# Kernel optimization log

Hardware: AMD Instinct MI355X
Metric: run time of the kernel (lower is better)

Reference implementation:

```python
import jax, jax.numpy as jnp
import numpy as np

N_PRED = 29
F_DIM = 8192
H1 = 256
H2 = 128


def setup_inputs() -> dict:
    key = jax.random.key(0)
    ks = jax.random.split(key, 7)
    features = jax.random.normal(ks[0], (4096, F_DIM), dtype=jnp.float32)
    # Stacked per-predicate MLP weights (PyTorch Linear init scale ~ 1/sqrt(fan_in))
    W1 = jax.random.normal(ks[1], (N_PRED, F_DIM, H1), dtype=jnp.float32) / np.sqrt(F_DIM)
    b1 = jax.random.normal(ks[2], (N_PRED, H1), dtype=jnp.float32) / np.sqrt(F_DIM)
    W2 = jax.random.normal(ks[3], (N_PRED, H1, H2), dtype=jnp.float32) / np.sqrt(H1)
    b2 = jax.random.normal(ks[4], (N_PRED, H2), dtype=jnp.float32) / np.sqrt(H1)
    W3 = jax.random.normal(ks[5], (N_PRED, H2), dtype=jnp.float32) / np.sqrt(H2)
    b3 = jax.random.normal(ks[6], (N_PRED,), dtype=jnp.float32) / np.sqrt(H2)
    return {"features": features, "W1": W1, "b1": b1, "W2": W2, "b2": b2, "W3": W3, "b3": b3}


def reference(features, W1, b1, W2, b2, W3, b3):
    # 29 parallel heads as one batched (grouped) GEMM chain; dropout = identity (eval).
    h1 = jax.nn.relu(jnp.einsum('bf,pfh->bph', features, W1) + b1[None])   # [B, P, H1]
    h2 = jax.nn.relu(jnp.einsum('bph,phk->bpk', h1, W2) + b2[None])        # [B, P, H2]
    logits = jnp.einsum('bpk,pk->bp', h2, W3) + b3[None]                   # [B, P]
    return jax.nn.sigmoid(logits)
```

## Files before the change

kernel.cpp:

```cpp
#include <hip/hip_runtime.h>
#include <hip/hip_bf16.h>

typedef __attribute__((ext_vector_type(8))) short short8_t;
typedef __attribute__((ext_vector_type(8))) __bf16 bf16x8;
typedef __attribute__((ext_vector_type(4))) float f32x4;

__device__ __forceinline__ void gload16(const void* g, void* l) {
  __builtin_amdgcn_global_load_lds(
      (const __attribute__((address_space(1))) void*)g,
      (__attribute__((address_space(3))) void*)l, 16, 0, 0);
}

__device__ __forceinline__ unsigned short f2bf(float f) {
  __hip_bfloat16 h = __float2bfloat16(f);
  return __builtin_bit_cast(unsigned short, h);
}

#define BARRIER() asm volatile("s_barrier" ::: "memory")


__global__ void k_cvt_feat(const float* __restrict__ in, unsigned short* __restrict__ out) {
  const size_t N = (size_t)4096 * 8192;
  size_t i = ((size_t)blockIdx.x * 256 + threadIdx.x) * 4;
  const size_t stride = (size_t)gridDim.x * 256 * 4;
  for (; i < N; i += stride) {
    float4 v = *(const float4*)(in + i);
    ushort4 o;
    o.x = f2bf(v.x); o.y = f2bf(v.y); o.z = f2bf(v.z); o.w = f2bf(v.w);
    *(ushort4*)(out + i) = o;
  }
}

__global__ void k_cvt_w1(const float* __restrict__ W1, unsigned short* __restrict__ out, int p0) {
  __shared__ unsigned short t[64][262];
  const int p = p0 + blockIdx.z;
  const float* src = W1 + (size_t)p * 8192 * 256;
  unsigned short* dst = out + (size_t)blockIdx.z * 256 * 8192;
  const int f0 = blockIdx.x * 256, h0 = blockIdx.y * 64;
#pragma unroll
  for (int i = 0; i < 64; ++i) {
    int tt = i * 256 + threadIdx.x;
    int f = tt >> 6, c = tt & 63;
    t[c][f] = f2bf(src[(size_t)(f0 + f) * 256 + h0 + c]);
  }
  __syncthreads();
#pragma unroll
  for (int i = 0; i < 8; ++i) {
    int tt = i * 256 + threadIdx.x;
    int r = tt >> 5;
    int c8 = (tt & 31) * 8;
    short8_t o;
#pragma unroll
    for (int j = 0; j < 8; ++j) o[j] = (short)t[r][c8 + j];
    *(short8_t*)&dst[(size_t)(h0 + r) * 8192 + f0 + c8] = o;
  }
}

__global__ void k_cvt_w2(const float* __restrict__ W2, unsigned short* __restrict__ out) {
  const int p = blockIdx.x;
  const float* src = W2 + (size_t)p * 256 * 128;
  unsigned short* dst = out + (size_t)p * 128 * 256;
  for (int tt = threadIdx.x; tt < 128 * 256; tt += 256) {
    int j = tt >> 8, h = tt & 255;
    dst[tt] = f2bf(src[(size_t)h * 128 + j]);
  }
}

__global__ __launch_bounds__(512, 2) void k_gemm1(
    const unsigned short* __restrict__ A,
    const unsigned short* __restrict__ Bt,
    const float* __restrict__ b1,
    const unsigned short* __restrict__ W2t,
    const float* __restrict__ b2,
    const float* __restrict__ W3,
    const float* __restrict__ b3,
    float* __restrict__ out,
    int p0) {
  __shared__ __align__(16) unsigned short S[65536];

  const int tid = threadIdx.x;
  const int lane = tid & 63;
  const int wave = tid >> 6;
  const int sr = (wave >> 2) * 64;
  const int sc = (wave & 3) * 32;

  const int nwg = gridDim.x * gridDim.y;
  const int orig = blockIdx.y * gridDim.x + blockIdx.x;
  const int q = nwg >> 3, r_ = nwg & 7;
  const int xcd = orig & 7, idx = orig >> 3;
  const int wg = (xcd < r_ ? xcd * (q + 1) : r_ * (q + 1) + (xcd - r_) * q) + idx;
  const int mx = wg & 15;
  const int z = wg >> 4;
  const int p = p0 + z;
  const int m0 = mx * 256;

  const unsigned short* Ab = A + (size_t)m0 * 8192;
  const unsigned short* Bb = Bt + (size_t)z * 256 * 8192;

  int e0 = tid, r0 = e0 >> 3, u0 = (e0 & 7) ^ (r0 & 7);
  int e1 = 512 + tid, r1e = e1 >> 3, u1 = (e1 & 7) ^ (r1e & 7);
  const size_t s0 = (size_t)r0 * 8192 + u0 * 8;
  const size_t s1 = (size_t)r1e * 8192 + u1 * 8;
  const int ld0 = (wave * 64) * 8;
  const int ld1 = (512 + wave * 64) * 8;

  auto stage = [&](int buf, int isB, int h, int T) {
    const unsigned short* gb = (isB ? Bb : Ab) + (size_t)h * 128 * 8192 + (size_t)T * 64;
    unsigned short* lb = S + buf * 32768 + isB * 16384 + h * 8192;
    gload16(gb + s0, lb + ld0);
    gload16(gb + s1, lb + ld1);
  };

  const int l15 = lane & 15, ks = lane >> 4;

  auto rdA = [&](int buf, int h, int mi, int x) {
    int R = sr + mi * 16 + l15;
    int pu = (x * 4 + ks) ^ (R & 7);
    return __builtin_bit_cast(bf16x8, *(const short8_t*)(S + buf * 32768 + h * 8192 + R * 64 + pu * 8));
  };
  auto rdB = [&](int buf, int v, int nj, int x) {
    int R = sc + nj * 16 + l15;
    int pu = (x * 4 + ks) ^ (R & 7);
    return __builtin_bit_cast(bf16x8, *(const short8_t*)(S + buf * 32768 + 16384 + v * 8192 + R * 64 + pu * 8));
  };

  f32x4 acc[4][4][2] = {};
  bf16x8 aH0[4][2], aH1[4][2], blf[2][2], bhf[2][2];
  const int NT = 8192 / 64;

  auto kstep = [&](int t, int pfa, int pf, int ra, int vm) {
    const int c = t & 1, nx = c ^ 1;
    BARRIER();
#pragma unroll
    for (int nj = 0; nj < 2; ++nj) { bhf[nj][0] = rdB(c, 1, nj, 0); bhf[nj][1] = rdB(c, 1, nj, 1); }
    if (pfa) stage(nx, 0, 1, t + 1);
    __builtin_amdgcn_s_setprio(1);
#pragma unroll
    for (int mi = 0; mi < 4; ++mi)
#pragma unroll
      for (int nj = 0; nj < 2; ++nj) {
        acc[0][mi][nj] = __builtin_amdgcn_mfma_f32_16x16x32_bf16(aH0[mi][0], blf[nj][0], acc[0][mi][nj], 0, 0, 0);
        acc[0][mi][nj] = __builtin_amdgcn_mfma_f32_16x16x32_bf16(aH0[mi][1], blf[nj][1], acc[0][mi][nj], 0, 0, 0);
      }
    __builtin_amdgcn_s_setprio(0);
    BARRIER();
#pragma unroll
    for (int mi = 0; mi < 4; ++mi) { aH1[mi][0] = rdA(c, 1, mi, 0); aH1[mi][1] = rdA(c, 1, mi, 1); }
    if (pf) stage(c, 0, 0, t + 2);
    __builtin_amdgcn_s_setprio(1);
#pragma unroll
    for (int mi = 0; mi < 4; ++mi)
#pragma unroll
      for (int nj = 0; nj < 2; ++nj) {
        acc[1][mi][nj] = __builtin_amdgcn_mfma_f32_16x16x32_bf16(aH0[mi][0], bhf[nj][0], acc[1][mi][nj], 0, 0, 0);
        acc[1][mi][nj] = __builtin_amdgcn_mfma_f32_16x16x32_bf16(aH0[mi][1], bhf[nj][1], acc[1][mi][nj], 0, 0, 0);
      }
    __builtin_amdgcn_s_setprio(0);
    BARRIER();
    if (pf) stage(c, 1, 1, t + 2);
    __builtin_amdgcn_s_setprio(1);
#pragma unroll
    for (int mi = 0; mi < 4; ++mi)
#pragma unroll
      for (int nj = 0; nj < 2; ++nj) {
        acc[2][mi][nj] = __builtin_amdgcn_mfma_f32_16x16x32_bf16(aH1[mi][0], blf[nj][0], acc[2][mi][nj], 0, 0, 0);
        acc[2][mi][nj] = __builtin_amdgcn_mfma_f32_16x16x32_bf16(aH1[mi][1], blf[nj][1], acc[2][mi][nj], 0, 0, 0);
      }
    __builtin_amdgcn_s_setprio(0);
    BARRIER();
    if (pf) stage(c, 1, 0, t + 2);
    if (vm == 6)      asm volatile("s_waitcnt vmcnt(6)" ::: "memory");
    else if (vm == 0) asm volatile("s_waitcnt vmcnt(0)" ::: "memory");
    BARRIER();
    if (ra) {
#pragma unroll
      for (int mi = 0; mi < 4; ++mi) { aH0[mi][0] = rdA(nx, 0, mi, 0); aH0[mi][1] = rdA(nx, 0, mi, 1); }
#pragma unroll
      for (int nj = 0; nj < 2; ++nj) { blf[nj][0] = rdB(nx, 0, nj, 0); blf[nj][1] = rdB(nx, 0, nj, 1); }
    }
    __builtin_amdgcn_s_setprio(1);
#pragma unroll
    for (int mi = 0; mi < 4; ++mi)
#pragma unroll
      for (int nj = 0; nj < 2; ++nj) {
        acc[3][mi][nj] = __builtin_amdgcn_mfma_f32_16x16x32_bf16(aH1[mi][0], bhf[nj][0], acc[3][mi][nj], 0, 0, 0);
        acc[3][mi][nj] = __builtin_amdgcn_mfma_f32_16x16x32_bf16(aH1[mi][1], bhf[nj][1], acc[3][mi][nj], 0, 0, 0);
      }
    __builtin_amdgcn_s_setprio(0);
  };

  stage(0, 0, 0, 0); stage(0, 1, 0, 0); stage(0, 1, 1, 0); stage(0, 0, 1, 0);
  stage(1, 0, 0, 1); stage(1, 1, 1, 1); stage(1, 1, 0, 1);
  asm volatile("s_waitcnt vmcnt(6)" ::: "memory");
  BARRIER();
#pragma unroll
  for (int mi = 0; mi < 4; ++mi) { aH0[mi][0] = rdA(0, 0, mi, 0); aH0[mi][1] = rdA(0, 0, mi, 1); }
#pragma unroll
  for (int nj = 0; nj < 2; ++nj) { blf[nj][0] = rdB(0, 0, nj, 0); blf[nj][1] = rdB(0, 0, nj, 1); }

  for (int t = 0; t < NT - 2; ++t) kstep(t, 1, 1, 1, 6);
  kstep(NT - 2, 1, 0, 1, 0);
  kstep(NT - 1, 0, 0, 0, -1);

  __syncthreads();
  {
    const int rg = lane >> 4;
#pragma unroll
    for (int qh = 0; qh < 2; ++qh)
#pragma unroll
      for (int qv = 0; qv < 2; ++qv) {
        const int qq = qh * 2 + qv;
#pragma unroll
        for (int nj = 0; nj < 2; ++nj) {
          const int c = qv * 128 + sc + nj * 16 + l15;
          const float bb = b1[p * 256 + c];
          const int u = c >> 3, sub = c & 7;
#pragma unroll
          for (int mi = 0; mi < 4; ++mi) {
            const int Rb = qh * 128 + sr + mi * 16 + rg * 4;
#pragma unroll
            for (int rr = 0; rr < 4; ++rr) {
              const int R = Rb + rr;
              float v = acc[qq][mi][nj][rr] + bb;
              v = v > 0.f ? v : 0.f;
              S[R * 256 + ((u ^ (R & 7)) * 8) + sub] = f2bf(v);
            }
          }
        }
      }
  }
  __syncthreads();
  {
    const unsigned short* Wp = W2t + (size_t)p * 128 * 256;
    f32x4 acc2[2][8] = {};
    bf16x8 bcur[8], bnxt[8];
#pragma unroll
    for (int nj = 0; nj < 8; ++nj)
      bcur[nj] = __builtin_bit_cast(bf16x8, *(const short8_t*)(Wp + (nj * 16 + l15) * 256 + ks * 8));
#pragma unroll
    for (int kt = 0; kt < 8; ++kt) {
      if (kt < 7) {
#pragma unroll
        for (int nj = 0; nj < 8; ++nj)
          bnxt[nj] = __builtin_bit_cast(bf16x8, *(const short8_t*)(Wp + (nj * 16 + l15) * 256 + (kt + 1) * 32 + ks * 8));
      }
      bf16x8 a2[2];
#pragma unroll
      for (int mi = 0; mi < 2; ++mi) {
        const int R = wave * 32 + mi * 16 + l15;
        const int u = kt * 4 + ks;
        a2[mi] = __builtin_bit_cast(bf16x8, *(const short8_t*)(S + R * 256 + ((u ^ (R & 7)) * 8)));
      }
#pragma unroll
      for (int mi = 0; mi < 2; ++mi)
#pragma unroll
        for (int nj = 0; nj < 8; ++nj)
          acc2[mi][nj] = __builtin_amdgcn_mfma_f32_16x16x32_bf16(a2[mi], bcur[nj], acc2[mi][nj], 0, 0, 0);
#pragma unroll
      for (int nj = 0; nj < 8; ++nj) bcur[nj] = bnxt[nj];
    }
    float b2v[8], w3v[8];
#pragma unroll
    for (int nj = 0; nj < 8; ++nj) {
      int c = nj * 16 + l15;
      b2v[nj] = b2[p * 128 + c];
      w3v[nj] = W3[p * 128 + c];
    }
    const float b3p = b3[p];
#pragma unroll
    for (int mi = 0; mi < 2; ++mi) {
#pragma unroll
      for (int r = 0; r < 4; ++r) {
        float s = 0.f;
#pragma unroll
        for (int nj = 0; nj < 8; ++nj) {
          float v = acc2[mi][nj][r] + b2v[nj];
          v = v > 0.f ? v : 0.f;
          s += v * w3v[nj];
        }
        s += __shfl_xor(s, 1);
        s += __shfl_xor(s, 2);
        s += __shfl_xor(s, 4);
        s += __shfl_xor(s, 8);
        if (l15 == 0) {
          int m = m0 + wave * 32 + mi * 16 + ks * 4 + r;
          float logit = s + b3p;
          out[(size_t)m * 29 + p] = 1.f / (1.f + __expf(-logit));
        }
      }
    }
  }
}

extern "C" void kernel_launch(void* const* d_in, const int* in_sizes, int n_in,
                              void* d_out, int out_size, void* d_ws, size_t ws_size,
                              hipStream_t stream) {
  const float* features = (const float*)d_in[0];
  const float* W1 = (const float*)d_in[1];
  const float* b1 = (const float*)d_in[2];
  const float* W2 = (const float*)d_in[3];
  const float* b2 = (const float*)d_in[4];
  const float* W3 = (const float*)d_in[5];
  const float* b3 = (const float*)d_in[6];
  float* out = (float*)d_out;

  char* ws = (char*)d_ws;
  const size_t featB = (size_t)4096 * 8192 * 2;
  const size_t w2B   = (size_t)29 * 128 * 256 * 2;
  const size_t w1pp  = (size_t)256 * 8192 * 2;

  unsigned short* featbf = (unsigned short*)ws;
  unsigned short* w2t    = (unsigned short*)(ws + featB);
  unsigned short* w1t    = (unsigned short*)(ws + featB + w2B);

  size_t base = featB + w2B;
  size_t rem = (ws_size > base) ? (ws_size - base) : 0;
  int CH = (int)(rem / w1pp);
  if (CH > 29) CH = 29;
  if (CH < 1) CH = 1;

  k_cvt_feat<<<2048, 256, 0, stream>>>(features, featbf);
  k_cvt_w2<<<29, 256, 0, stream>>>(W2, w2t);

  for (int p0 = 0; p0 < 29; p0 += CH) {
    int c = (29 - p0) < CH ? (29 - p0) : CH;
    k_cvt_w1<<<dim3(32, 4, c), 256, 0, stream>>>(W1, w1t, p0);
    k_gemm1<<<dim3(16, c), 512, 0, stream>>>(featbf, w1t, b1, w2t, b2, W3, b3, out, p0);
  }
}
```

Measured before the change: 531.8 us.

## Switch layer-1 GEMM to 32x32x16 MFMA with k-major LDS layout

Replaces the 16x16x32 bf16 MFMA tiles in the main W1 GEMM with 32x32x16 MFMA, which cuts the instruction count and raises operand reuse per instruction. The LDS staging layout changes from a row-major XOR-swizzled layout to a k-chunk-major layout so that 32-row fragments can be read contiguously. The epilogue is rewritten to match the 32x32 accumulator register mapping. The unswizzled layout may bring LDS bank conflicts on writes or reads, and the strided global loads may coalesce less well.

```diff
diff --git a/kernel.cpp b/kernel.cpp
--- a/kernel.cpp
+++ b/kernel.cpp
@@ -4,6 +4,7 @@
 typedef __attribute__((ext_vector_type(8))) short short8_t;
 typedef __attribute__((ext_vector_type(8))) __bf16 bf16x8;
 typedef __attribute__((ext_vector_type(4))) float f32x4;
+typedef __attribute__((ext_vector_type(16))) float f32x16;
 
 __device__ __forceinline__ void gload16(const void* g, void* l) {
   __builtin_amdgcn_global_load_lds(
@@ -97,8 +98,8 @@
   const unsigned short* Ab = A + (size_t)m0 * 8192;
   const unsigned short* Bb = Bt + (size_t)z * 256 * 8192;
 
-  int e0 = tid, r0 = e0 >> 3, u0 = (e0 & 7) ^ (r0 & 7);
-  int e1 = 512 + tid, r1e = e1 >> 3, u1 = (e1 & 7) ^ (r1e & 7);
+  int e0 = tid, u0 = e0 >> 7, r0 = e0 & 127;
+  int e1 = 512 + tid, u1 = e1 >> 7, r1e = e1 & 127;
   const size_t s0 = (size_t)r0 * 8192 + u0 * 8;
   const size_t s1 = (size_t)r1e * 8192 + u1 * 8;
   const int ld0 = (wave * 64) * 8;
@@ -112,60 +113,57 @@
   };
 
   const int l15 = lane & 15, ks = lane >> 4;
-
-  auto rdA = [&](int buf, int h, int mi, int x) {
-    int R = sr + mi * 16 + l15;
-    int pu = (x * 4 + ks) ^ (R & 7);
-    return __builtin_bit_cast(bf16x8, *(const short8_t*)(S + buf * 32768 + h * 8192 + R * 64 + pu * 8));
+  const int l31 = lane & 31, ks2 = lane >> 5;
+
+  auto rdA = [&](int buf, int h, int mi2, int kx) {
+    int R = sr + mi2 * 32 + l31;
+    int u = kx * 2 + ks2;
+    return __builtin_bit_cast(bf16x8, *(const short8_t*)(S + buf * 32768 + h * 8192 + u * 1024 + R * 8));
   };
-  auto rdB = [&](int buf, int v, int nj, int x) {
-    int R = sc + nj * 16 + l15;
-    int pu = (x * 4 + ks) ^ (R & 7);
-    return __builtin_bit_cast(bf16x8, *(const short8_t*)(S + buf * 32768 + 16384 + v * 8192 + R * 64 + pu * 8));
+  auto rdB = [&](int buf, int v, int kx) {
+    int R = sc + l31;
+    int u = kx * 2 + ks2;
+    return __builtin_bit_cast(bf16x8, *(const short8_t*)(S + buf * 32768 + 16384 + v * 8192 + u * 1024 + R * 8));
   };
 
-  f32x4 acc[4][4][2] = {};
-  bf16x8 aH0[4][2], aH1[4][2], blf[2][2], bhf[2][2];
+  f32x16 acc[4][2] = {};
+  bf16x8 aH0[2][4], aH1[2][4], blf[4], bhf[4];
   const int NT = 8192 / 64;
 
   auto kstep = [&](int t, int pfa, int pf, int ra, int vm) {
     const int c = t & 1, nx = c ^ 1;
     BARRIER();
 #pragma unroll
-    for (int nj = 0; nj < 2; ++nj) { bhf[nj][0] = rdB(c, 1, nj, 0); bhf[nj][1] = rdB(c, 1, nj, 1); }
+    for (int kx = 0; kx < 4; ++kx) bhf[kx] = rdB(c, 1, kx);
     if (pfa) stage(nx, 0, 1, t + 1);
     __builtin_amdgcn_s_setprio(1);
 #pragma unroll
-    for (int mi = 0; mi < 4; ++mi)
-#pragma unroll
-      for (int nj = 0; nj < 2; ++nj) {
-        acc[0][mi][nj] = __builtin_amdgcn_mfma_f32_16x16x32_bf16(aH0[mi][0], blf[nj][0], acc[0][mi][nj], 0, 0, 0);
-        acc[0][mi][nj] = __builtin_amdgcn_mfma_f32_16x16x32_bf16(aH0[mi][1], blf[nj][1], acc[0][mi][nj], 0, 0, 0);
-      }
+    for (int kx = 0; kx < 4; ++kx)
+#pragma unroll
+      for (int mi2 = 0; mi2 < 2; ++mi2)
+        acc[0][mi2] = __builtin_amdgcn_mfma_f32_32x32x16_bf16(aH0[mi2][kx], blf[kx], acc[0][mi2], 0, 0, 0);
     __builtin_amdgcn_s_setprio(0);
     BARRIER();
 #pragma unroll
-    for (int mi = 0; mi < 4; ++mi) { aH1[mi][0] = rdA(c, 1, mi, 0); aH1[mi][1] = rdA(c, 1, mi, 1); }
+    for (int mi2 = 0; mi2 < 2; ++mi2)
+#pragma unroll
+      for (int kx = 0; kx < 4; ++kx) aH1[mi2][kx] = rdA(c, 1, mi2, kx);
     if (pf) stage(c, 0, 0, t + 2);
     __builtin_amdgcn_s_setprio(1);
 #pragma unroll
-    for (int mi = 0; mi < 4; ++mi)
-#pragma unroll
-      for (int nj = 0; nj < 2; ++nj) {
-        acc[1][mi][nj] = __builtin_amdgcn_mfma_f32_16x16x32_bf16(aH0[mi][0], bhf[nj][0], acc[1][mi][nj], 0, 0, 0);
-        acc[1][mi][nj] = __builtin_amdgcn_mfma_f32_16x16x32_bf16(aH0[mi][1], bhf[nj][1], acc[1][mi][nj], 0, 0, 0);
-      }
+    for (int kx = 0; kx < 4; ++kx)
+#pragma unroll
+      for (int mi2 = 0; mi2 < 2; ++mi2)
+        acc[1][mi2] = __builtin_amdgcn_mfma_f32_32x32x16_bf16(aH0[mi2][kx], bhf[kx], acc[1][mi2], 0, 0, 0);
     __builtin_amdgcn_s_setprio(0);
     BARRIER();
     if (pf) stage(c, 1, 1, t + 2);
     __builtin_amdgcn_s_setprio(1);
 #pragma unroll
-    for (int mi = 0; mi < 4; ++mi)
-#pragma unroll
-      for (int nj = 0; nj < 2; ++nj) {
-        acc[2][mi][nj] = __builtin_amdgcn_mfma_f32_16x16x32_bf16(aH1[mi][0], blf[nj][0], acc[2][mi][nj], 0, 0, 0);
-        acc[2][mi][nj] = __builtin_amdgcn_mfma_f32_16x16x32_bf16(aH1[mi][1], blf[nj][1], acc[2][mi][nj], 0, 0, 0);
-      }
+    for (int kx = 0; kx < 4; ++kx)
+#pragma unroll
+      for (int mi2 = 0; mi2 < 2; ++mi2)
+        acc[2][mi2] = __builtin_amdgcn_mfma_f32_32x32x16_bf16(aH1[mi2][kx], blf[kx], acc[2][mi2], 0, 0, 0);
     __builtin_amdgcn_s_setprio(0);
     BARRIER();
     if (pf) stage(c, 1, 0, t + 2);
@@ -174,18 +172,18 @@
     BARRIER();
     if (ra) {
 #pragma unroll
-      for (int mi = 0; mi < 4; ++mi) { aH0[mi][0] = rdA(nx, 0, mi, 0); aH0[mi][1] = rdA(nx, 0, mi, 1); }
-#pragma unroll
-      for (int nj = 0; nj < 2; ++nj) { blf[nj][0] = rdB(nx, 0, nj, 0); blf[nj][1] = rdB(nx, 0, nj, 1); }
+      for (int mi2 = 0; mi2 < 2; ++mi2)
+#pragma unroll
+        for (int kx = 0; kx < 4; ++kx) aH0[mi2][kx] = rdA(nx, 0, mi2, kx);
+#pragma unroll
+      for (int kx = 0; kx < 4; ++kx) blf[kx] = rdB(nx, 0, kx);
     }
     __builtin_amdgcn_s_setprio(1);
 #pragma unroll
-    for (int mi = 0; mi < 4; ++mi)
-#pragma unroll
-      for (int nj = 0; nj < 2; ++nj) {
-        acc[3][mi][nj] = __builtin_amdgcn_mfma_f32_16x16x32_bf16(aH1[mi][0], bhf[nj][0], acc[3][mi][nj], 0, 0, 0);
-        acc[3][mi][nj] = __builtin_amdgcn_mfma_f32_16x16x32_bf16(aH1[mi][1], bhf[nj][1], acc[3][mi][nj], 0, 0, 0);
-      }
+    for (int kx = 0; kx < 4; ++kx)
+#pragma unroll
+      for (int mi2 = 0; mi2 < 2; ++mi2)
+        acc[3][mi2] = __builtin_amdgcn_mfma_f32_32x32x16_bf16(aH1[mi2][kx], bhf[kx], acc[3][mi2], 0, 0, 0);
     __builtin_amdgcn_s_setprio(0);
   };
 
@@ -194,9 +192,11 @@
   asm volatile("s_waitcnt vmcnt(6)" ::: "memory");
   BARRIER();
 #pragma unroll
-  for (int mi = 0; mi < 4; ++mi) { aH0[mi][0] = rdA(0, 0, mi, 0); aH0[mi][1] = rdA(0, 0, mi, 1); }
-#pragma unroll
-  for (int nj = 0; nj < 2; ++nj) { blf[nj][0] = rdB(0, 0, nj, 0); blf[nj][1] = rdB(0, 0, nj, 1); }
+  for (int mi2 = 0; mi2 < 2; ++mi2)
+#pragma unroll
+    for (int kx = 0; kx < 4; ++kx) aH0[mi2][kx] = rdA(0, 0, mi2, kx);
+#pragma unroll
+  for (int kx = 0; kx < 4; ++kx) blf[kx] = rdB(0, 0, kx);
 
   for (int t = 0; t < NT - 2; ++t) kstep(t, 1, 1, 1, 6);
   kstep(NT - 2, 1, 0, 1, 0);
@@ -204,27 +204,23 @@
 
   __syncthreads();
   {
-    const int rg = lane >> 4;
 #pragma unroll
     for (int qh = 0; qh < 2; ++qh)
 #pragma unroll
       for (int qv = 0; qv < 2; ++qv) {
         const int qq = qh * 2 + qv;
-#pragma unroll
-        for (int nj = 0; nj < 2; ++nj) {
-          const int c = qv * 128 + sc + nj * 16 + l15;
-          const float bb = b1[p * 256 + c];
-          const int u = c >> 3, sub = c & 7;
-#pragma unroll
-          for (int mi = 0; mi < 4; ++mi) {
-            const int Rb = qh * 128 + sr + mi * 16 + rg * 4;
-#pragma unroll
-            for (int rr = 0; rr < 4; ++rr) {
-              const int R = Rb + rr;
-              float v = acc[qq][mi][nj][rr] + bb;
-              v = v > 0.f ? v : 0.f;
-              S[R * 256 + ((u ^ (R & 7)) * 8) + sub] = f2bf(v);
-            }
+        const int col = qv * 128 + sc + l31;
+        const float bb = b1[p * 256 + col];
+        const int u = col >> 3, sub = col & 7;
+#pragma unroll
+        for (int mi2 = 0; mi2 < 2; ++mi2) {
+          const int Rb = qh * 128 + sr + mi2 * 32 + 4 * ks2;
+#pragma unroll
+          for (int rg = 0; rg < 16; ++rg) {
+            const int R = Rb + (rg & 3) + 8 * (rg >> 2);
+            float v = acc[qq][mi2][rg] + bb;
+            v = v > 0.f ? v : 0.f;
+            S[R * 256 + ((u ^ (R & 7)) * 8) + sub] = f2bf(v);
           }
         }
       }
```

After: 703.9 us. 32.4% more time.
